# Kernel tuning notes

Measured on AMD Instinct MI355X. Metric: run time of the kernel, lower is better.

## Reference

```python
import jax, jax.numpy as jnp
import numpy as np
import math

DIM = 512
BLOCK_NUM = 16
SEQ_LEN = 8192
BLOCK_LEN = SEQ_LEN // BLOCK_NUM  # 512 == DIM -> mask used as-is
BATCH = 4
LN_EPS = 1e-3  # keras LayerNormalization default epsilon


def setup_inputs() -> dict:
    key = jax.random.key(0)
    ks = jax.random.split(key, 5)
    inputs = jax.random.normal(ks[0], (BATCH, BLOCK_NUM, BLOCK_LEN, DIM), dtype=jnp.float32)
    # binary padding-style mask, values in {0,1}
    mask_array = jax.random.randint(ks[1], (BATCH, SEQ_LEN, DIM), 0, 2).astype(jnp.float32)
    scale = 1.0 / math.sqrt(DIM)
    dw1 = jax.random.normal(ks[2], (DIM, DIM), dtype=jnp.float32) * scale
    dw2 = jax.random.normal(ks[3], (DIM, DIM), dtype=jnp.float32) * scale
    dw3 = jax.random.normal(ks[4], (DIM, DIM), dtype=jnp.float32) * scale
    db1 = jnp.zeros((DIM,), dtype=jnp.float32)
    db2 = jnp.zeros((DIM,), dtype=jnp.float32)
    db3 = jnp.zeros((DIM,), dtype=jnp.float32)
    return {"inputs": inputs, "mask_array": mask_array,
            "dw1": dw1, "dw2": dw2, "dw3": dw3,
            "db1": db1, "db2": db2, "db3": db3}


def reference(inputs, mask_array, dw1, dw2, dw3, db1, db2, db3):
    # inputs: [B, block_num, block_len, dim]
    Q = jnp.matmul(inputs, dw1) + db1
    K = jnp.matmul(inputs, dw2) + db2
    V = jnpp_matmul = jnp.matmul(inputs, dw3) + db3
    V = jnp.matmul(inputs, dw3) + db3
    # block-local attention scores: [B, bn, bl, bl]
    scores = jnp.einsum('bnqd,bnkd->bnqk', Q, K) / math.sqrt(DIM)
    # mask: [B, seq_len, dim] -> [B, bn, bl, dim]; block_len == dim so no slice/tile
    m = mask_array.reshape(BATCH, BLOCK_NUM, BLOCK_LEN, DIM)
    scores = scores + (1.0 - m) * jnp.float32(-1e10)
    p = jax.nn.softmax(scores, axis=-1)
    out = jnp.einsum('bnqk,bnkd->bnqd', p, V) + inputs  # residual
    # LayerNorm(axis=-1), fresh keras layer: gamma=1, beta=0, eps=1e-3
    mean = jnp.mean(out, axis=-1, keepdims=True)
    var = jnp.mean(jnp.square(out - mean), axis=-1, keepdims=True)
    return (out - mean) / jnp.sqrt(var + LN_EPS)
```

## Files before the change

### kernel.cpp

```cpp
#include <hip/hip_runtime.h>

#define DIMK 512
#define NBLK 64
#define NTOK 32768

typedef short  short8 __attribute__((ext_vector_type(8)));
typedef float  f32x4  __attribute__((ext_vector_type(4)));
typedef unsigned short u16x8 __attribute__((ext_vector_type(8)));

__device__ __forceinline__ unsigned short f2bf(float f) {
  union { float f; unsigned u; } v; v.f = f;
  unsigned r = (v.u + 0x7FFFu + ((v.u >> 16) & 1u)) >> 16;
  return (unsigned short)r;
}
__device__ __forceinline__ float bf2f(unsigned short h) {
  return __uint_as_float(((unsigned)h) << 16);
}

__device__ __forceinline__ void gload_lds16(const unsigned short* g,
                                            unsigned short* l) {
  __builtin_amdgcn_global_load_lds(
      (const __attribute__((address_space(1))) unsigned int*)(g),
      (__attribute__((address_space(3))) unsigned int*)(l),
      16, 0, 0);
}

__device__ __forceinline__ int swz(int c) { return c ^ ((c >> 3) & 3); }


__global__ __launch_bounds__(256) void k_prep(
    const float* __restrict__ X, const float* __restrict__ mask,
    const float* __restrict__ dw1, const float* __restrict__ dw2,
    const float* __restrict__ dw3,
    unsigned short* __restrict__ Xb, unsigned char* __restrict__ bits,
    unsigned short* __restrict__ Wt)
{
  __shared__ float t[64][65];
  const int b = blockIdx.x;
  const int tid = threadIdx.x;
  if (b < 8192) {
    const size_t gid = (size_t)b * 256 + tid;
    const size_t i = gid * 8;
    const int tok = (int)(i >> 9);
    const int col = (int)(i & 511);
    const float4 a = *(const float4*)(X + i);
    const float4 bb = *(const float4*)(X + i + 4);
    u16x8 o;
    o[0] = f2bf(a.x); o[1] = f2bf(a.y); o[2] = f2bf(a.z); o[3] = f2bf(a.w);
    o[4] = f2bf(bb.x); o[5] = f2bf(bb.y); o[6] = f2bf(bb.z); o[7] = f2bf(bb.w);
    *(u16x8*)(Xb + ((size_t)(tok >> 7) * 16 + (col >> 5)) * 4096 +
              (tok & 127) * 32 + (col & 31)) = o;
  } else if (b < 16384) {
    const size_t gid = (size_t)(b - 8192) * 256 + tid;
    const size_t i = gid * 8;
    const float4 ma = *(const float4*)(mask + i);
    const float4 mb = *(const float4*)(mask + i + 4);
    unsigned v = 0;
    v |= (ma.x > 0.5f) << 0; v |= (ma.y > 0.5f) << 1;
    v |= (ma.z > 0.5f) << 2; v |= (ma.w > 0.5f) << 3;
    v |= (mb.x > 0.5f) << 4; v |= (mb.y > 0.5f) << 5;
    v |= (mb.z > 0.5f) << 6; v |= (mb.w > 0.5f) << 7;
    bits[gid] = (unsigned char)v;
  } else {
    const int bb = b - 16384;
    const int w = bb >> 6;
    const int tt = bb & 63;
    const int kt = (tt >> 3) * 64;
    const int nt = (tt & 7) * 64;
    const float* dw = (w == 0) ? dw1 : (w == 1) ? dw2 : dw3;
    const int rr = tid >> 4;
    const int cc = (tid & 15) << 2;
#pragma unroll
    for (int p = 0; p < 4; ++p) {
      const int r = rr + p * 16;
      const float4 v = *(const float4*)&dw[(size_t)(kt + r) * 512 + nt + cc];
      t[cc + 0][r] = v.x; t[cc + 1][r] = v.y;
      t[cc + 2][r] = v.z; t[cc + 3][r] = v.w;
    }
    __syncthreads();
#pragma unroll
    for (int p = 0; p < 4; ++p) {
      const int r = rr + p * 16;
      const int n = nt + r;
      const int k = kt + cc;
      ushort4 o;
      o.x = f2bf(t[r][cc + 0]); o.y = f2bf(t[r][cc + 1]);
      o.z = f2bf(t[r][cc + 2]); o.w = f2bf(t[r][cc + 3]);
      *(ushort4*)&Wt[(size_t)w * 262144 + (size_t)(k >> 5) * 16384 +
                     (size_t)n * 32 + (k & 31)] = o;
    }
  }
}

__global__ __launch_bounds__(256, 2) void k_qkv(
    const unsigned short* __restrict__ Xb, const unsigned short* __restrict__ Wt,
    const float* __restrict__ db1, const float* __restrict__ db2,
    const float* __restrict__ db3,
    unsigned short* __restrict__ Qb, unsigned short* __restrict__ Kb,
    unsigned short* __restrict__ Vt)
{
  __shared__ __align__(16) unsigned short smem[32768];

  const int id = blockIdx.x;
  const int x = id & 7, j = id >> 3;
  const int mtile = x * 32 + (j >> 2);
  const int nt = j & 3;
  const int m0 = mtile * 128;
  const int n0 = nt * 128;

  const int tid = threadIdx.x, lane = tid & 63, wv = tid >> 6;
  const int quad = lane >> 4, l16 = lane & 15;
  const int qx = quad ^ ((l16 >> 1) & 3);
  const int rb = (wv >> 1) * 64, cb = (wv & 1) * 64;

  f32x4 acc[3][4][4];
#pragma unroll
  for (int w = 0; w < 3; ++w)
#pragma unroll
    for (int i = 0; i < 4; ++i)
#pragma unroll
      for (int jj = 0; jj < 4; ++jj) {
        f32x4 z = {0.f, 0.f, 0.f, 0.f}; acc[w][i][jj] = z;
      }

  auto stage = [&](unsigned short* base, int it) {
    const unsigned short* aslab = Xb + ((size_t)mtile * 16 + it) * 4096;
    gload_lds16(aslab + swz(tid) * 8, base + tid * 8);
    gload_lds16(aslab + swz(tid + 256) * 8, base + (tid + 256) * 8);
#pragma unroll
    for (int h = 0; h < 6; ++h) {
      const int c = tid + h * 256;
      const int w = c >> 9, cc = c & 511;
      const unsigned short* bslab =
          Wt + (size_t)w * 262144 + (size_t)it * 16384 + (size_t)n0 * 32;
      gload_lds16(bslab + swz(cc) * 8, base + 4096 + w * 4096 + cc * 8);
    }
  };

  stage(smem, 0);
  __syncthreads();
  int cur = 0;
  for (int it = 0; it < 16; ++it) {
    unsigned short* cbuf = smem + cur * 16384;
    if (it < 15) stage(smem + (cur ^ 1) * 16384, it + 1);
    const unsigned short* As = cbuf;
    const unsigned short* Bs = cbuf + 4096;
    short8 af[4];
#pragma unroll
    for (int i = 0; i < 4; ++i)
      af[i] = *(const short8*)&As[(rb + i * 16 + l16) * 32 + qx * 8];
#pragma unroll
    for (int jj = 0; jj < 4; ++jj)
#pragma unroll
      for (int w = 0; w < 3; ++w) {
        const short8 bf =
            *(const short8*)&Bs[w * 4096 + (cb + jj * 16 + l16) * 32 + qx * 8];
#pragma unroll
        for (int i = 0; i < 4; ++i)
          acc[w][i][jj] = __builtin_amdgcn_mfma_f32_16x16x32_bf16(
              af[i], bf, acc[w][i][jj], 0, 0, 0);
      }
    __syncthreads();
    cur ^= 1;
  }

#pragma unroll
  for (int i = 0; i < 4; ++i)
#pragma unroll
    for (int jj = 0; jj < 4; ++jj)
#pragma unroll
      for (int r = 0; r < 4; ++r) {
        const int tok = m0 + rb + i * 16 + quad * 4 + r;
        const int col = n0 + cb + jj * 16 + l16;
        Qb[((size_t)(tok >> 6) * 16 + (col >> 5)) * 2048 +
           (tok & 63) * 32 + (col & 31)] = f2bf(acc[0][i][jj][r] + db1[col]);
        Kb[((size_t)(tok >> 9) * 16 + (col >> 5)) * 16384 +
           (tok & 511) * 32 + (col & 31)] = f2bf(acc[1][i][jj][r] + db2[col]);
      }
#pragma unroll
  for (int i = 0; i < 4; ++i)
#pragma unroll
    for (int jj = 0; jj < 4; ++jj) {
      const int cl = cb + jj * 16 + l16;
      const int t0 = rb + i * 16 + quad * 4;
      const float bv = db3[n0 + cl];
      ushort4 pk;
      pk.x = f2bf(acc[2][i][jj][0] + bv);
      pk.y = f2bf(acc[2][i][jj][1] + bv);
      pk.z = f2bf(acc[2][i][jj][2] + bv);
      pk.w = f2bf(acc[2][i][jj][3] + bv);
      *(ushort4*)&smem[cl * 136 + t0] = pk;
    }
  __syncthreads();
#pragma unroll
  for (int h = 0; h < 8; ++h) {
    const int c = tid + h * 256;
    const int cl = c >> 4, toff = (c & 15) * 8;
    const int tg = mtile * 128 + toff;
    *(u16x8*)&Vt[(size_t)(tg >> 5) * 16384 + (size_t)(n0 + cl) * 32 +
                 (tg & 31)] = *(const u16x8*)&smem[cl * 136 + toff];
  }
}

__global__ __launch_bounds__(256, 2) void k_attn_p(
    const unsigned short* __restrict__ Qb, const unsigned short* __restrict__ Kb,
    const unsigned long long* __restrict__ bits, unsigned short* __restrict__ Pb)
{
  __shared__ __align__(16) unsigned short smem[36864];
  __shared__ float red[4][64];
  const int tid = threadIdx.x, lane = tid & 63, wv = tid >> 6;
  const int quad = lane >> 4, l16 = lane & 15;
  const int qx = quad ^ ((l16 >> 1) & 3);
  const int blk = blockIdx.x & 63, mt = blockIdx.x >> 6;
  const size_t q0 = (size_t)blk * 512 + (size_t)mt * 64;
  const int qt = blk * 8 + mt;

  f32x4 acc[4][8];
#pragma unroll
  for (int i = 0; i < 4; ++i)
#pragma unroll
    for (int j = 0; j < 8; ++j) { f32x4 z = {0.f, 0.f, 0.f, 0.f}; acc[i][j] = z; }

  auto stage = [&](unsigned short* base, int it) {
    const unsigned short* aslab = Qb + ((size_t)qt * 16 + it) * 2048;
    gload_lds16(aslab + swz(tid) * 8, base + tid * 8);
    const unsigned short* bslab = Kb + ((size_t)blk * 16 + it) * 16384;
#pragma unroll
    for (int h = 0; h < 8; ++h) {
      const int c = tid + h * 256;
      gload_lds16(bslab + swz(c) * 8, base + 2048 + c * 8);
    }
  };

  stage(smem, 0);
  __syncthreads();
  int cur = 0;
  for (int it = 0; it < 16; ++it) {
    unsigned short* cbuf = smem + cur * 18432;
    if (it < 15) stage(smem + (cur ^ 1) * 18432, it + 1);
    const unsigned short* As = cbuf;
    const unsigned short* Bs = cbuf + 2048;
    short8 af[4], bfv[8];
#pragma unroll
    for (int i = 0; i < 4; ++i)
      af[i] = *(const short8*)&As[(i * 16 + l16) * 32 + qx * 8];
#pragma unroll
    for (int j = 0; j < 8; ++j)
      bfv[j] = *(const short8*)&Bs[(wv * 128 + j * 16 + l16) * 32 + qx * 8];
#pragma unroll
    for (int i = 0; i < 4; ++i)
#pragma unroll
      for (int j = 0; j < 8; ++j)
        acc[i][j] = __builtin_amdgcn_mfma_f32_16x16x32_bf16(
            af[i], bfv[j], acc[i][j], 0, 0, 0);
    __syncthreads();
    cur ^= 1;
  }

  const float scale = 0.04419417382415922f;
  float rmax[4][4];
#pragma unroll
  for (int i = 0; i < 4; ++i)
#pragma unroll
    for (int r = 0; r < 4; ++r) rmax[i][r] = -3.0e38f;
#pragma unroll
  for (int i = 0; i < 4; ++i)
#pragma unroll
    for (int r = 0; r < 4; ++r) {
      const size_t tok = q0 + i * 16 + quad * 4 + r;
      const unsigned long long w0 = bits[tok * 8 + wv * 2];
      const unsigned long long w1 = bits[tok * 8 + wv * 2 + 1];
#pragma unroll
      for (int j = 0; j < 8; ++j) {
        const unsigned long long sel = (j < 4) ? w0 : w1;
        const float bias = ((sel >> (l16 + 16 * (j & 3))) & 1ull) ? 0.0f : -1e10f;
        const float v = acc[i][j][r] * scale + bias;
        acc[i][j][r] = v;
        rmax[i][r] = fmaxf(rmax[i][r], v);
      }
    }
#pragma unroll
  for (int i = 0; i < 4; ++i)
#pragma unroll
    for (int r = 0; r < 4; ++r)
      for (int d = 1; d < 16; d <<= 1)
        rmax[i][r] = fmaxf(rmax[i][r], __shfl_xor(rmax[i][r], d, 64));
  if (l16 == 0)
#pragma unroll
    for (int i = 0; i < 4; ++i)
#pragma unroll
      for (int r = 0; r < 4; ++r) red[wv][i * 16 + quad * 4 + r] = rmax[i][r];
  __syncthreads();
#pragma unroll
  for (int i = 0; i < 4; ++i)
#pragma unroll
    for (int r = 0; r < 4; ++r) {
      const int row = i * 16 + quad * 4 + r;
      rmax[i][r] = fmaxf(fmaxf(red[0][row], red[1][row]),
                         fmaxf(red[2][row], red[3][row]));
    }
  __syncthreads();
  float rsum[4][4];
#pragma unroll
  for (int i = 0; i < 4; ++i)
#pragma unroll
    for (int r = 0; r < 4; ++r) rsum[i][r] = 0.f;
#pragma unroll
  for (int i = 0; i < 4; ++i)
#pragma unroll
    for (int j = 0; j < 8; ++j)
#pragma unroll
      for (int r = 0; r < 4; ++r) {
        const float e = __expf(acc[i][j][r] - rmax[i][r]);
        acc[i][j][r] = e;
        rsum[i][r] += e;
      }
#pragma unroll
  for (int i = 0; i < 4; ++i)
#pragma unroll
    for (int r = 0; r < 4; ++r)
      for (int d = 1; d < 16; d <<= 1)
        rsum[i][r] += __shfl_xor(rsum[i][r], d, 64);
  if (l16 == 0)
#pragma unroll
    for (int i = 0; i < 4; ++i)
#pragma unroll
      for (int r = 0; r < 4; ++r) red[wv][i * 16 + quad * 4 + r] = rsum[i][r];
  __syncthreads();
#pragma unroll
  for (int i = 0; i < 4; ++i)
#pragma unroll
    for (int r = 0; r < 4; ++r) {
      const int row = i * 16 + quad * 4 + r;
      rsum[i][r] = 1.0f / (red[0][row] + red[1][row] + red[2][row] + red[3][row]);
    }
#pragma unroll
  for (int i = 0; i < 4; ++i)
#pragma unroll
    for (int j = 0; j < 8; ++j)
#pragma unroll
      for (int r = 0; r < 4; ++r) {
        const int tok = (int)(q0 + i * 16 + quad * 4 + r);
        const int col = wv * 128 + j * 16 + l16;
        Pb[((size_t)(tok >> 6) * 16 + (col >> 5)) * 2048 +
           (tok & 63) * 32 + (col & 31)] = f2bf(acc[i][j][r] * rsum[i][r]);
      }
}

__global__ __launch_bounds__(256, 2) void k_pv_ln(
    const unsigned short* __restrict__ Pb, const unsigned short* __restrict__ Vt,
    const unsigned short* __restrict__ Xb, float* __restrict__ Out)
{
  __shared__ __align__(16) unsigned short smem[36864];
  __shared__ float2 red[4][64];
  const int tid = threadIdx.x, lane = tid & 63, wv = tid >> 6;
  const int quad = lane >> 4, l16 = lane & 15;
  const int qx = quad ^ ((l16 >> 1) & 3);
  const int blk = blockIdx.x & 63, mt = blockIdx.x >> 6;
  const size_t q0 = (size_t)blk * 512 + (size_t)mt * 64;
  const int qt = blk * 8 + mt;

  f32x4 acc[4][8];
#pragma unroll
  for (int i = 0; i < 4; ++i)
#pragma unroll
    for (int j = 0; j < 8; ++j) { f32x4 z = {0.f, 0.f, 0.f, 0.f}; acc[i][j] = z; }

  auto stage = [&](unsigned short* base, int it) {
    const unsigned short* aslab = Pb + ((size_t)qt * 16 + it) * 2048;
    gload_lds16(aslab + swz(tid) * 8, base + tid * 8);
    const unsigned short* bslab = Vt + ((size_t)blk * 16 + it) * 16384;
#pragma unroll
    for (int h = 0; h < 8; ++h) {
      const int c = tid + h * 256;
      gload_lds16(bslab + swz(c) * 8, base + 2048 + c * 8);
    }
  };

  stage(smem, 0);
  __syncthreads();
  int cur = 0;
  for (int it = 0; it < 16; ++it) {
    unsigned short* cbuf = smem + cur * 18432;
    if (it < 15) stage(smem + (cur ^ 1) * 18432, it + 1);
    const unsigned short* As = cbuf;
    const unsigned short* Bs = cbuf + 2048;
    short8 af[4], bfv[8];
#pragma unroll
    for (int i = 0; i < 4; ++i)
      af[i] = *(const short8*)&As[(i * 16 + l16) * 32 + qx * 8];
#pragma unroll
    for (int j = 0; j < 8; ++j)
      bfv[j] = *(const short8*)&Bs[(wv * 128 + j * 16 + l16) * 32 + qx * 8];
#pragma unroll
    for (int i = 0; i < 4; ++i)
#pragma unroll
      for (int j = 0; j < 8; ++j)
        acc[i][j] = __builtin_amdgcn_mfma_f32_16x16x32_bf16(
            af[i], bfv[j], acc[i][j], 0, 0, 0);
    __syncthreads();
    cur ^= 1;
  }

  float vsum[4][4], vsq[4][4];
#pragma unroll
  for (int i = 0; i < 4; ++i)
#pragma unroll
    for (int r = 0; r < 4; ++r) { vsum[i][r] = 0.f; vsq[i][r] = 0.f; }
#pragma unroll
  for (int i = 0; i < 4; ++i)
#pragma unroll
    for (int j = 0; j < 8; ++j)
#pragma unroll
      for (int r = 0; r < 4; ++r) {
        const int tok = (int)(q0 + i * 16 + quad * 4 + r);
        const int col = wv * 128 + j * 16 + l16;
        const float v = acc[i][j][r] +
            bf2f(Xb[((size_t)(tok >> 7) * 16 + (col >> 5)) * 4096 +
                    (tok & 127) * 32 + (col & 31)]);
        acc[i][j][r] = v;
        vsum[i][r] += v;
        vsq[i][r] += v * v;
      }
#pragma unroll
  for (int i = 0; i < 4; ++i)
#pragma unroll
    for (int r = 0; r < 4; ++r)
      for (int d = 1; d < 16; d <<= 1) {
        vsum[i][r] += __shfl_xor(vsum[i][r], d, 64);
        vsq[i][r]  += __shfl_xor(vsq[i][r], d, 64);
      }
  if (l16 == 0)
#pragma unroll
    for (int i = 0; i < 4; ++i)
#pragma unroll
      for (int r = 0; r < 4; ++r) {
        float2 p; p.x = vsum[i][r]; p.y = vsq[i][r];
        red[wv][i * 16 + quad * 4 + r] = p;
      }
  __syncthreads();
#pragma unroll
  for (int i = 0; i < 4; ++i)
#pragma unroll
    for (int r = 0; r < 4; ++r) {
      const int row = i * 16 + quad * 4 + r;
      float s = 0.f, q = 0.f;
#pragma unroll
      for (int w = 0; w < 4; ++w) { s += red[w][row].x; q += red[w][row].y; }
      const float mean = s * (1.0f / 512.0f);
      const float var  = q * (1.0f / 512.0f) - mean * mean;
      vsum[i][r] = mean;
      vsq[i][r]  = rsqrtf(var + 1e-3f);
    }
#pragma unroll
  for (int i = 0; i < 4; ++i)
#pragma unroll
    for (int j = 0; j < 8; ++j)
#pragma unroll
      for (int r = 0; r < 4; ++r) {
        const size_t tok = q0 + i * 16 + quad * 4 + r;
        const int col = wv * 128 + j * 16 + l16;
        Out[tok * (size_t)DIMK + col] =
            (acc[i][j][r] - vsum[i][r]) * vsq[i][r];
      }
}

extern "C" void kernel_launch(void* const* d_in, const int* in_sizes, int n_in,
                              void* d_out, int out_size, void* d_ws, size_t ws_size,
                              hipStream_t stream)
{
  const float* X    = (const float*)d_in[0];
  const float* mask = (const float*)d_in[1];
  const float* dw1  = (const float*)d_in[2];
  const float* dw2  = (const float*)d_in[3];
  const float* dw3  = (const float*)d_in[4];
  const float* db1  = (const float*)d_in[5];
  const float* db2  = (const float*)d_in[6];
  const float* db3  = (const float*)d_in[7];
  float* Out = (float*)d_out;

  char* ws = (char*)d_ws;
  const size_t MB = 1ull << 20;
  unsigned short* Wt = (unsigned short*)(ws);
  unsigned short* Qb = (unsigned short*)(ws + 2 * MB);
  unsigned short* Kb = (unsigned short*)(ws + 34 * MB);
  unsigned short* Vt = (unsigned short*)(ws + 66 * MB);
  unsigned short* Xb = (unsigned short*)(ws + 98 * MB);
  unsigned short* Pb = Qb;
  unsigned char*  bits = (unsigned char*)d_out;

  k_prep   <<<16576, 256, 0, stream>>>(X, mask, dw1, dw2, dw3, Xb, bits, Wt);
  k_qkv    <<<1024, 256, 0, stream>>>(Xb, Wt, db1, db2, db3, Qb, Kb, Vt);
  k_attn_p <<<512, 256, 0, stream>>>(Qb, Kb, (const unsigned long long*)bits, Pb);
  k_pv_ln  <<<512, 256, 0, stream>>>(Pb, Vt, Xb, Out);
}
```

Baseline: 295.6 us.

## Replace LDS double-buffered staging with direct global fragment loads in GEMM kernels

Removes the global_load_lds double-buffered staging, swizzle and per-iteration barriers from the QKV, QK^T and PV kernels. MFMA operand fragments are now loaded directly from global memory, relying on L1/L2 cache for reuse. This drops barrier and LDS traffic and frees LDS, which may raise occupancy. In exchange, each wave reissues global loads for shared operand tiles and loses the overlap of prefetch with compute, so the loop may become latency bound.

```diff
diff --git a/kernel.cpp b/kernel.cpp
--- a/kernel.cpp
+++ b/kernel.cpp
@@ -16,16 +16,6 @@
 __device__ __forceinline__ float bf2f(unsigned short h) {
   return __uint_as_float(((unsigned)h) << 16);
 }
-
-__device__ __forceinline__ void gload_lds16(const unsigned short* g,
-                                            unsigned short* l) {
-  __builtin_amdgcn_global_load_lds(
-      (const __attribute__((address_space(1))) unsigned int*)(g),
-      (__attribute__((address_space(3))) unsigned int*)(l),
-      16, 0, 0);
-}
-
-__device__ __forceinline__ int swz(int c) { return c ^ ((c >> 3) & 3); }
 
 
 __global__ __launch_bounds__(256) void k_prep(
@@ -99,7 +89,7 @@
     unsigned short* __restrict__ Qb, unsigned short* __restrict__ Kb,
     unsigned short* __restrict__ Vt)
 {
-  __shared__ __align__(16) unsigned short smem[32768];
+  __shared__ __align__(16) unsigned short smem[128 * 136];
 
   const int id = blockIdx.x;
   const int x = id & 7, j = id >> 3;
@@ -110,7 +100,6 @@
 
   const int tid = threadIdx.x, lane = tid & 63, wv = tid >> 6;
   const int quad = lane >> 4, l16 = lane & 15;
-  const int qx = quad ^ ((l16 >> 1) & 3);
   const int rb = (wv >> 1) * 64, cb = (wv & 1) * 64;
 
   f32x4 acc[3][4][4];
@@ -123,45 +112,27 @@
         f32x4 z = {0.f, 0.f, 0.f, 0.f}; acc[w][i][jj] = z;
       }
 
-  auto stage = [&](unsigned short* base, int it) {
+  for (int it = 0; it < 16; ++it) {
     const unsigned short* aslab = Xb + ((size_t)mtile * 16 + it) * 4096;
-    gload_lds16(aslab + swz(tid) * 8, base + tid * 8);
-    gload_lds16(aslab + swz(tid + 256) * 8, base + (tid + 256) * 8);
-#pragma unroll
-    for (int h = 0; h < 6; ++h) {
-      const int c = tid + h * 256;
-      const int w = c >> 9, cc = c & 511;
+    short8 af[4];
+#pragma unroll
+    for (int i = 0; i < 4; ++i)
+      af[i] = *(const short8*)&aslab[(rb + i * 16 + l16) * 32 + quad * 8];
+#pragma unroll
+    for (int w = 0; w < 3; ++w) {
       const unsigned short* bslab =
           Wt + (size_t)w * 262144 + (size_t)it * 16384 + (size_t)n0 * 32;
-      gload_lds16(bslab + swz(cc) * 8, base + 4096 + w * 4096 + cc * 8);
-    }
-  };
-
-  stage(smem, 0);
-  __syncthreads();
-  int cur = 0;
-  for (int it = 0; it < 16; ++it) {
-    unsigned short* cbuf = smem + cur * 16384;
-    if (it < 15) stage(smem + (cur ^ 1) * 16384, it + 1);
-    const unsigned short* As = cbuf;
-    const unsigned short* Bs = cbuf + 4096;
-    short8 af[4];
-#pragma unroll
-    for (int i = 0; i < 4; ++i)
-      af[i] = *(const short8*)&As[(rb + i * 16 + l16) * 32 + qx * 8];
-#pragma unroll
-    for (int jj = 0; jj < 4; ++jj)
-#pragma unroll
-      for (int w = 0; w < 3; ++w) {
-        const short8 bf =
-            *(const short8*)&Bs[w * 4096 + (cb + jj * 16 + l16) * 32 + qx * 8];
+      short8 bf[4];
+#pragma unroll
+      for (int jj = 0; jj < 4; ++jj)
+        bf[jj] = *(const short8*)&bslab[(cb + jj * 16 + l16) * 32 + quad * 8];
+#pragma unroll
+      for (int jj = 0; jj < 4; ++jj)
 #pragma unroll
         for (int i = 0; i < 4; ++i)
           acc[w][i][jj] = __builtin_amdgcn_mfma_f32_16x16x32_bf16(
-              af[i], bf, acc[w][i][jj], 0, 0, 0);
-      }
-    __syncthreads();
-    cur ^= 1;
+              af[i], bf[jj], acc[w][i][jj], 0, 0, 0);
+    }
   }
 
 #pragma unroll
@@ -206,11 +177,9 @@
     const unsigned short* __restrict__ Qb, const unsigned short* __restrict__ Kb,
     const unsigned long long* __restrict__ bits, unsigned short* __restrict__ Pb)
 {
-  __shared__ __align__(16) unsigned short smem[36864];
   __shared__ float red[4][64];
   const int tid = threadIdx.x, lane = tid & 63, wv = tid >> 6;
   const int quad = lane >> 4, l16 = lane & 15;
-  const int qx = quad ^ ((l16 >> 1) & 3);
   const int blk = blockIdx.x & 63, mt = blockIdx.x >> 6;
   const size_t q0 = (size_t)blk * 512 + (size_t)mt * 64;
   const int qt = blk * 8 + mt;
@@ -221,40 +190,22 @@
 #pragma unroll
     for (int j = 0; j < 8; ++j) { f32x4 z = {0.f, 0.f, 0.f, 0.f}; acc[i][j] = z; }
 
-  auto stage = [&](unsigned short* base, int it) {
+  for (int it = 0; it < 16; ++it) {
     const unsigned short* aslab = Qb + ((size_t)qt * 16 + it) * 2048;
-    gload_lds16(aslab + swz(tid) * 8, base + tid * 8);
     const unsigned short* bslab = Kb + ((size_t)blk * 16 + it) * 16384;
-#pragma unroll
-    for (int h = 0; h < 8; ++h) {
-      const int c = tid + h * 256;
-      gload_lds16(bslab + swz(c) * 8, base + 2048 + c * 8);
-    }
-  };
-
-  stage(smem, 0);
-  __syncthreads();
-  int cur = 0;
-  for (int it = 0; it < 16; ++it) {
-    unsigned short* cbuf = smem + cur * 18432;
-    if (it < 15) stage(smem + (cur ^ 1) * 18432, it + 1);
-    const unsigned short* As = cbuf;
-    const unsigned short* Bs = cbuf + 2048;
     short8 af[4], bfv[8];
 #pragma unroll
     for (int i = 0; i < 4; ++i)
-      af[i] = *(const short8*)&As[(i * 16 + l16) * 32 + qx * 8];
-#pragma unroll
-    for (int j = 0; j < 8; ++j)
-      bfv[j] = *(const short8*)&Bs[(wv * 128 + j * 16 + l16) * 32 + qx * 8];
+      af[i] = *(const short8*)&aslab[(i * 16 + l16) * 32 + quad * 8];
+#pragma unroll
+    for (int j = 0; j < 8; ++j)
+      bfv[j] = *(const short8*)&bslab[(wv * 128 + j * 16 + l16) * 32 + quad * 8];
 #pragma unroll
     for (int i = 0; i < 4; ++i)
 #pragma unroll
       for (int j = 0; j < 8; ++j)
         acc[i][j] = __builtin_amdgcn_mfma_f32_16x16x32_bf16(
             af[i], bfv[j], acc[i][j], 0, 0, 0);
-    __syncthreads();
-    cur ^= 1;
   }
 
   const float scale = 0.04419417382415922f;
@@ -351,11 +302,9 @@
     const unsigned short* __restrict__ Pb, const unsigned short* __restrict__ Vt,
     const unsigned short* __restrict__ Xb, float* __restrict__ Out)
 {
-  __shared__ __align__(16) unsigned short smem[36864];
   __shared__ float2 red[4][64];
   const int tid = threadIdx.x, lane = tid & 63, wv = tid >> 6;
   const int quad = lane >> 4, l16 = lane & 15;
-  const int qx = quad ^ ((l16 >> 1) & 3);
   const int blk = blockIdx.x & 63, mt = blockIdx.x >> 6;
   const size_t q0 = (size_t)blk * 512 + (size_t)mt * 64;
   const int qt = blk * 8 + mt;
@@ -366,40 +315,22 @@
 #pragma unroll
     for (int j = 0; j < 8; ++j) { f32x4 z = {0.f, 0.f, 0.f, 0.f}; acc[i][j] = z; }
 
-  auto stage = [&](unsigned short* base, int it) {
+  for (int it = 0; it < 16; ++it) {
     const unsigned short* aslab = Pb + ((size_t)qt * 16 + it) * 2048;
-    gload_lds16(aslab + swz(tid) * 8, base + tid * 8);
     const unsigned short* bslab = Vt + ((size_t)blk * 16 + it) * 16384;
-#pragma unroll
-    for (int h = 0; h < 8; ++h) {
-      const int c = tid + h * 256;
-      gload_lds16(bslab + swz(c) * 8, base + 2048 + c * 8);
-    }
-  };
-
-  stage(smem, 0);
-  __syncthreads();
-  int cur = 0;
-  for (int it = 0; it < 16; ++it) {
-    unsigned short* cbuf = smem + cur * 18432;
-    if (it < 15) stage(smem + (cur ^ 1) * 18432, it + 1);
-    const unsigned short* As = cbuf;
-    const unsigned short* Bs = cbuf + 2048;
     short8 af[4], bfv[8];
 #pragma unroll
     for (int i = 0; i < 4; ++i)
-      af[i] = *(const short8*)&As[(i * 16 + l16) * 32 + qx * 8];
-#pragma unroll
-    for (int j = 0; j < 8; ++j)
-      bfv[j] = *(const short8*)&Bs[(wv * 128 + j * 16 + l16) * 32 + qx * 8];
+      af[i] = *(const short8*)&aslab[(i * 16 + l16) * 32 + quad * 8];
+#pragma unroll
+    for (int j = 0; j < 8; ++j)
+      bfv[j] = *(const short8*)&bslab[(wv * 128 + j * 16 + l16) * 32 + quad * 8];
 #pragma unroll
     for (int i = 0; i < 4; ++i)
 #pragma unroll
       for (int j = 0; j < 8; ++j)
         acc[i][j] = __builtin_amdgcn_mfma_f32_16x16x32_bf16(
             af[i], bfv[j], acc[i][j], 0, 0, 0);
-    __syncthreads();
-    cur ^= 1;
   }
 
   float vsum[4][4], vsq[4][4];
```

New measurement: 339.9 us. +15.0%, slower.

## Enlarge attention tiles to 128 rows with triple-buffered LDS pipeline

Applied to the files above, without the earlier changes.

Both attention kernels (QK^T+softmax and PV+LayerNorm) now use 512-thread blocks with 8 waves in a 2x4 layout. Each block covers 128 query rows instead of 64, so every K/V slab staged into LDS is reused across twice as many rows, halving redundant global traffic for the shared operand. The double buffer with __syncthreads is replaced by a 3-stage LDS ring with explicit vmcnt waits and a single barrier per iteration, so loads run two steps ahead. Block IDs are also remapped to interleave attention blocks. LDS use rises to about 127KB per block, which limits residency to one block per CU and halves the grid to 256 blocks, so there are fewer blocks to hide latency.

```diff
diff --git a/kernel.cpp b/kernel.cpp
--- a/kernel.cpp
+++ b/kernel.cpp
@@ -202,18 +202,21 @@
   }
 }
 
-__global__ __launch_bounds__(256, 2) void k_attn_p(
+__global__ __launch_bounds__(512, 2) void k_attn_p(
     const unsigned short* __restrict__ Qb, const unsigned short* __restrict__ Kb,
     const unsigned long long* __restrict__ bits, unsigned short* __restrict__ Pb)
 {
-  __shared__ __align__(16) unsigned short smem[36864];
-  __shared__ float red[4][64];
+  __shared__ __align__(16) unsigned short smem[61440];
+  __shared__ float red[4][128];
   const int tid = threadIdx.x, lane = tid & 63, wv = tid >> 6;
+  const int wr = wv >> 2, wc = wv & 3;
   const int quad = lane >> 4, l16 = lane & 15;
   const int qx = quad ^ ((l16 >> 1) & 3);
-  const int blk = blockIdx.x & 63, mt = blockIdx.x >> 6;
-  const size_t q0 = (size_t)blk * 512 + (size_t)mt * 64;
-  const int qt = blk * 8 + mt;
+  const int id = blockIdx.x;
+  const int blk = (id & 7) * 8 + ((id >> 3) & 7);
+  const int mt = id >> 6;
+  const size_t q0 = (size_t)blk * 512 + (size_t)mt * 128;
+  const int qt0 = blk * 8 + mt * 2;
 
   f32x4 acc[4][8];
 #pragma unroll
@@ -221,40 +224,41 @@
 #pragma unroll
     for (int j = 0; j < 8; ++j) { f32x4 z = {0.f, 0.f, 0.f, 0.f}; acc[i][j] = z; }
 
-  auto stage = [&](unsigned short* base, int it) {
-    const unsigned short* aslab = Qb + ((size_t)qt * 16 + it) * 2048;
-    gload_lds16(aslab + swz(tid) * 8, base + tid * 8);
+  auto stage = [&](int it) {
+    unsigned short* base = smem + (it % 3) * 20480;
+    const unsigned short* aslab =
+        Qb + ((size_t)(qt0 + (tid >> 8)) * 16 + it) * 2048;
+    gload_lds16(aslab + swz(tid & 255) * 8, base + tid * 8);
     const unsigned short* bslab = Kb + ((size_t)blk * 16 + it) * 16384;
 #pragma unroll
-    for (int h = 0; h < 8; ++h) {
-      const int c = tid + h * 256;
-      gload_lds16(bslab + swz(c) * 8, base + 2048 + c * 8);
+    for (int h = 0; h < 4; ++h) {
+      const int c = tid + h * 512;
+      gload_lds16(bslab + swz(c) * 8, base + 4096 + c * 8);
     }
   };
 
-  stage(smem, 0);
-  __syncthreads();
-  int cur = 0;
+  stage(0);
+  stage(1);
   for (int it = 0; it < 16; ++it) {
-    unsigned short* cbuf = smem + cur * 18432;
-    if (it < 15) stage(smem + (cur ^ 1) * 18432, it + 1);
-    const unsigned short* As = cbuf;
-    const unsigned short* Bs = cbuf + 2048;
+    if (it < 15) asm volatile("s_waitcnt vmcnt(5)" ::: "memory");
+    else         asm volatile("s_waitcnt vmcnt(0)" ::: "memory");
+    __builtin_amdgcn_s_barrier();
+    if (it + 2 < 16) stage(it + 2);
+    const unsigned short* As = smem + (it % 3) * 20480;
+    const unsigned short* Bs = As + 4096;
     short8 af[4], bfv[8];
 #pragma unroll
     for (int i = 0; i < 4; ++i)
-      af[i] = *(const short8*)&As[(i * 16 + l16) * 32 + qx * 8];
+      af[i] = *(const short8*)&As[(wr * 64 + i * 16 + l16) * 32 + qx * 8];
 #pragma unroll
     for (int j = 0; j < 8; ++j)
-      bfv[j] = *(const short8*)&Bs[(wv * 128 + j * 16 + l16) * 32 + qx * 8];
+      bfv[j] = *(const short8*)&Bs[(wc * 128 + j * 16 + l16) * 32 + qx * 8];
 #pragma unroll
     for (int i = 0; i < 4; ++i)
 #pragma unroll
       for (int j = 0; j < 8; ++j)
         acc[i][j] = __builtin_amdgcn_mfma_f32_16x16x32_bf16(
             af[i], bfv[j], acc[i][j], 0, 0, 0);
-    __syncthreads();
-    cur ^= 1;
   }
 
   const float scale = 0.04419417382415922f;
@@ -267,9 +271,9 @@
   for (int i = 0; i < 4; ++i)
 #pragma unroll
     for (int r = 0; r < 4; ++r) {
-      const size_t tok = q0 + i * 16 + quad * 4 + r;
-      const unsigned long long w0 = bits[tok * 8 + wv * 2];
-      const unsigned long long w1 = bits[tok * 8 + wv * 2 + 1];
+      const size_t tok = q0 + wr * 64 + i * 16 + quad * 4 + r;
+      const unsigned long long w0 = bits[tok * 8 + wc * 2];
+      const unsigned long long w1 = bits[tok * 8 + wc * 2 + 1];
 #pragma unroll
       for (int j = 0; j < 8; ++j) {
         const unsigned long long sel = (j < 4) ? w0 : w1;
@@ -289,13 +293,14 @@
 #pragma unroll
     for (int i = 0; i < 4; ++i)
 #pragma unroll
-      for (int r = 0; r < 4; ++r) red[wv][i * 16 + quad * 4 + r] = rmax[i][r];
+      for (int r = 0; r < 4; ++r)
+        red[wc][wr * 64 + i * 16 + quad * 4 + r] = rmax[i][r];
   __syncthreads();
 #pragma unroll
   for (int i = 0; i < 4; ++i)
 #pragma unroll
     for (int r = 0; r < 4; ++r) {
-      const int row = i * 16 + quad * 4 + r;
+      const int row = wr * 64 + i * 16 + quad * 4 + r;
       rmax[i][r] = fmaxf(fmaxf(red[0][row], red[1][row]),
                          fmaxf(red[2][row], red[3][row]));
     }
@@ -325,13 +330,14 @@
 #pragma unroll
     for (int i = 0; i < 4; ++i)
 #pragma unroll
-      for (int r = 0; r < 4; ++r) red[wv][i * 16 + quad * 4 + r] = rsum[i][r];
+      for (int r = 0; r < 4; ++r)
+        red[wc][wr * 64 + i * 16 + quad * 4 + r] = rsum[i][r];
   __syncthreads();
 #pragma unroll
   for (int i = 0; i < 4; ++i)
 #pragma unroll
     for (int r = 0; r < 4; ++r) {
-      const int row = i * 16 + quad * 4 + r;
+      const int row = wr * 64 + i * 16 + quad * 4 + r;
       rsum[i][r] = 1.0f / (red[0][row] + red[1][row] + red[2][row] + red[3][row]);
     }
 #pragma unroll
@@ -340,25 +346,28 @@
     for (int j = 0; j < 8; ++j)
 #pragma unroll
       for (int r = 0; r < 4; ++r) {
-        const int tok = (int)(q0 + i * 16 + quad * 4 + r);
-        const int col = wv * 128 + j * 16 + l16;
+        const int tok = (int)(q0 + wr * 64 + i * 16 + quad * 4 + r);
+        const int col = wc * 128 + j * 16 + l16;
         Pb[((size_t)(tok >> 6) * 16 + (col >> 5)) * 2048 +
            (tok & 63) * 32 + (col & 31)] = f2bf(acc[i][j][r] * rsum[i][r]);
       }
 }
 
-__global__ __launch_bounds__(256, 2) void k_pv_ln(
+__global__ __launch_bounds__(512, 2) void k_pv_ln(
     const unsigned short* __restrict__ Pb, const unsigned short* __restrict__ Vt,
     const unsigned short* __restrict__ Xb, float* __restrict__ Out)
 {
-  __shared__ __align__(16) unsigned short smem[36864];
-  __shared__ float2 red[4][64];
+  __shared__ __align__(16) unsigned short smem[61440];
+  __shared__ float2 red[4][128];
   const int tid = threadIdx.x, lane = tid & 63, wv = tid >> 6;
+  const int wr = wv >> 2, wc = wv & 3;
   const int quad = lane >> 4, l16 = lane & 15;
   const int qx = quad ^ ((l16 >> 1) & 3);
-  const int blk = blockIdx.x & 63, mt = blockIdx.x >> 6;
-  const size_t q0 = (size_t)blk * 512 + (size_t)mt * 64;
-  const int qt = blk * 8 + mt;
+  const int id = blockIdx.x;
+  const int blk = (id & 7) * 8 + ((id >> 3) & 7);
+  const int mt = id >> 6;
+  const size_t q0 = (size_t)blk * 512 + (size_t)mt * 128;
+  const int qt0 = blk * 8 + mt * 2;
 
   f32x4 acc[4][8];
 #pragma unroll
@@ -366,40 +375,41 @@
 #pragma unroll
     for (int j = 0; j < 8; ++j) { f32x4 z = {0.f, 0.f, 0.f, 0.f}; acc[i][j] = z; }
 
-  auto stage = [&](unsigned short* base, int it) {
-    const unsigned short* aslab = Pb + ((size_t)qt * 16 + it) * 2048;
-    gload_lds16(aslab + swz(tid) * 8, base + tid * 8);
+  auto stage = [&](int it) {
+    unsigned short* base = smem + (it % 3) * 20480;
+    const unsigned short* aslab =
+        Pb + ((size_t)(qt0 + (tid >> 8)) * 16 + it) * 2048;
+    gload_lds16(aslab + swz(tid & 255) * 8, base + tid * 8);
     const unsigned short* bslab = Vt + ((size_t)blk * 16 + it) * 16384;
 #pragma unroll
-    for (int h = 0; h < 8; ++h) {
-      const int c = tid + h * 256;
-      gload_lds16(bslab + swz(c) * 8, base + 2048 + c * 8);
+    for (int h = 0; h < 4; ++h) {
+      const int c = tid + h * 512;
+      gload_lds16(bslab + swz(c) * 8, base + 4096 + c * 8);
     }
   };
 
-  stage(smem, 0);
-  __syncthreads();
-  int cur = 0;
+  stage(0);
+  stage(1);
   for (int it = 0; it < 16; ++it) {
-    unsigned short* cbuf = smem + cur * 18432;
-    if (it < 15) stage(smem + (cur ^ 1) * 18432, it + 1);
-    const unsigned short* As = cbuf;
-    const unsigned short* Bs = cbuf + 2048;
+    if (it < 15) asm volatile("s_waitcnt vmcnt(5)" ::: "memory");
+    else         asm volatile("s_waitcnt vmcnt(0)" ::: "memory");
+    __builtin_amdgcn_s_barrier();
+    if (it + 2 < 16) stage(it + 2);
+    const unsigned short* As = smem + (it % 3) * 20480;
+    const unsigned short* Bs = As + 4096;
     short8 af[4], bfv[8];
 #pragma unroll
     for (int i = 0; i < 4; ++i)
-      af[i] = *(const short8*)&As[(i * 16 + l16) * 32 + qx * 8];
+      af[i] = *(const short8*)&As[(wr * 64 + i * 16 + l16) * 32 + qx * 8];
 #pragma unroll
     for (int j = 0; j < 8; ++j)
-      bfv[j] = *(const short8*)&Bs[(wv * 128 + j * 16 + l16) * 32 + qx * 8];
+      bfv[j] = *(const short8*)&Bs[(wc * 128 + j * 16 + l16) * 32 + qx * 8];
 #pragma unroll
     for (int i = 0; i < 4; ++i)
 #pragma unroll
       for (int j = 0; j < 8; ++j)
         acc[i][j] = __builtin_amdgcn_mfma_f32_16x16x32_bf16(
             af[i], bfv[j], acc[i][j], 0, 0, 0);
-    __syncthreads();
-    cur ^= 1;
   }
 
   float vsum[4][4], vsq[4][4];
@@ -413,8 +423,8 @@
     for (int j = 0; j < 8; ++j)
 #pragma unroll
       for (int r = 0; r < 4; ++r) {
-        const int tok = (int)(q0 + i * 16 + quad * 4 + r);
-        const int col = wv * 128 + j * 16 + l16;
+        const int tok = (int)(q0 + wr * 64 + i * 16 + quad * 4 + r);
+        const int col = wc * 128 + j * 16 + l16;
         const float v = acc[i][j][r] +
             bf2f(Xb[((size_t)(tok >> 7) * 16 + (col >> 5)) * 4096 +
                     (tok & 127) * 32 + (col & 31)]);
@@ -436,14 +446,14 @@
 #pragma unroll
       for (int r = 0; r < 4; ++r) {
         float2 p; p.x = vsum[i][r]; p.y = vsq[i][r];
-        red[wv][i * 16 + quad * 4 + r] = p;
+        red[wc][wr * 64 + i * 16 + quad * 4 + r] = p;
       }
   __syncthreads();
 #pragma unroll
   for (int i = 0; i < 4; ++i)
 #pragma unroll
     for (int r = 0; r < 4; ++r) {
-      const int row = i * 16 + quad * 4 + r;
+      const int row = wr * 64 + i * 16 + quad * 4 + r;
       float s = 0.f, q = 0.f;
 #pragma unroll
       for (int w = 0; w < 4; ++w) { s += red[w][row].x; q += red[w][row].y; }
@@ -458,8 +468,8 @@
     for (int j = 0; j < 8; ++j)
 #pragma unroll
       for (int r = 0; r < 4; ++r) {
-        const size_t tok = q0 + i * 16 + quad * 4 + r;
-        const int col = wv * 128 + j * 16 + l16;
+        const size_t tok = q0 + wr * 64 + i * 16 + quad * 4 + r;
+        const int col = wc * 128 + j * 16 + l16;
         Out[tok * (size_t)DIMK + col] =
             (acc[i][j][r] - vsum[i][r]) * vsq[i][r];
       }
@@ -491,6 +501,6 @@
 
   k_prep   <<<16576, 256, 0, stream>>>(X, mask, dw1, dw2, dw3, Xb, bits, Wt);
   k_qkv    <<<1024, 256, 0, stream>>>(Xb, Wt, db1, db2, db3, Qb, Kb, Vt);
-  k_attn_p <<<512, 256, 0, stream>>>(Qb, Kb, (const unsigned long long*)bits, Pb);
-  k_pv_ln  <<<512, 256, 0, stream>>>(Pb, Vt, Xb, Out);
-}
+  k_attn_p <<<256, 512, 0, stream>>>(Qb, Kb, (const unsigned long long*)bits, Pb);
+  k_pv_ln  <<<256, 512, 0, stream>>>(Pb, Vt, Xb, Out);
+}
```

Result: no change. 298.3 us (+0.9%).
